# Optimization experiments

Measured on AMD Instinct MI355X. Metric: run time of the kernel, lower is better.

Reference implementation:

```python
import jax, jax.numpy as jnp
import numpy as np

T, H, I, E, K = 4096, 2048, 2048, 16, 4
EPS = 1e-6


def setup_inputs() -> dict:
    key = jax.random.key(0)
    ks = jax.random.split(key, 7)
    s = 0.02
    return {
        "x": jax.random.normal(ks[0], (T, H), dtype=jnp.float32),
        "gamma": jnp.ones((H,), dtype=jnp.float32),
        "wg": jax.random.normal(ks[1], (E, H), dtype=jnp.float32) * s,
        "bg": jax.random.normal(ks[2], (E,), dtype=jnp.float32) * s,
        "w1": jax.random.normal(ks[3], (E, I, H), dtype=jnp.float32) * s,  # gate proj
        "w3": jax.random.normal(ks[4], (E, I, H), dtype=jnp.float32) * s,  # up proj
        "w2": jax.random.normal(ks[5], (E, H, I), dtype=jnp.float32) * s,  # down proj
    }


def reference(x, gamma, wg, bg, w1, w3, w2):
    # RMSNorm
    t = x * jax.lax.rsqrt(jnp.mean(x * x, axis=-1, keepdims=True) + EPS) * gamma
    # Router: softmax -> top-k -> renormalize (FusedMoE renormalize=True)
    logits = t @ wg.T + bg                        # [T, E]
    probs = jax.nn.softmax(logits, axis=-1)
    vals, idx = jax.lax.top_k(probs, K)           # [T, K]
    vals = vals / jnp.sum(vals, axis=-1, keepdims=True)
    # Dense [T, E] routing-weight matrix (zeros outside top-k)
    route_w = jnp.einsum("tk,tke->te", vals, jax.nn.one_hot(idx, E, dtype=vals.dtype))
    # Grouped expert GEMMs: scan over experts, accumulate weighted outputs
    def body(acc, p):
        w1e, w3e, w2e, we = p                     # [I,H], [I,H], [H,I], [T]
        h = jax.nn.silu(t @ w1e.T) * (t @ w3e.T)  # [T, I]
        return acc + (h @ w2e.T) * we[:, None], None
    moe_out, _ = jax.lax.scan(body, jnp.zeros_like(x), (w1, w3, w2, route_w.T))
    return x + moe_out
```

## Files before the change

kernel.cpp:

```cpp
#include <hip/hip_runtime.h>
#include <hip/hip_bf16.h>

constexpr int TT = 4096;
constexpr int HH = 2048;
constexpr int II = 2048;
constexpr int EE = 16;
constexpr int KTOP = 4;

typedef __attribute__((ext_vector_type(4))) float f4;
typedef __attribute__((ext_vector_type(8))) short s8;

__device__ __forceinline__ short f2bf(float f) {
    union { __hip_bfloat16 b; short s; } u;
    u.b = __float2bfloat16(f);
    return u.s;
}
__device__ __forceinline__ float bf2f(short s) {
    union { unsigned u; float f; } v;
    v.u = ((unsigned)(unsigned short)s) << 16;
    return v.f;
}

__global__ void k_router(const float* __restrict__ x, const float* __restrict__ gamma,
                         const float* __restrict__ wg, const float* __restrict__ bg,
                         short* __restrict__ t16, int* __restrict__ cnt,
                         int* __restrict__ lst, float* __restrict__ lwt) {
    const int lane = threadIdx.x & 63;
    const int tok = blockIdx.x * 4 + (threadIdx.x >> 6);
    const float* xr = x + (size_t)tok * HH;
    float t[32];
    float ss = 0.f;
#pragma unroll
    for (int j = 0; j < 32; j++) { float v = xr[lane + 64 * j]; t[j] = v; ss += v * v; }
#pragma unroll
    for (int m = 32; m >= 1; m >>= 1) ss += __shfl_xor(ss, m);
    const float rs = rsqrtf(ss * (1.f / HH) + 1e-6f);
#pragma unroll
    for (int j = 0; j < 32; j++) t[j] *= rs * gamma[lane + 64 * j];

    short* tr = t16 + (size_t)tok * HH;
#pragma unroll
    for (int j = 0; j < 32; j++) tr[lane + 64 * j] = f2bf(t[j]);

    float logit[EE];
#pragma unroll
    for (int e = 0; e < EE; e++) {
        const float* wrow = wg + (size_t)e * HH;
        float a = 0.f;
#pragma unroll
        for (int j = 0; j < 32; j++) a += t[j] * wrow[lane + 64 * j];
#pragma unroll
        for (int m = 32; m >= 1; m >>= 1) a += __shfl_xor(a, m);
        logit[e] = a + bg[e];
    }
    unsigned chosen = 0u;
    int sel[KTOP]; float sv[KTOP];
#pragma unroll
    for (int k = 0; k < KTOP; k++) {
        float best = -1e30f; int bi = 0;
#pragma unroll
        for (int e = 0; e < EE; e++) {
            bool take = (!((chosen >> e) & 1u)) && (logit[e] > best);
            if (take) { best = logit[e]; bi = e; }
        }
        chosen |= 1u << bi; sel[k] = bi; sv[k] = best;
    }
    const float lmax = sv[0];
    float s = 0.f;
#pragma unroll
    for (int k = 0; k < KTOP; k++) { sv[k] = expf(sv[k] - lmax); s += sv[k]; }
    const float inv = 1.f / s;
    if (lane == 0) {
#pragma unroll
        for (int k = 0; k < KTOP; k++) {
            int e = sel[k];
            int p = atomicAdd(&cnt[e], 1);
            lst[e * TT + p] = tok * KTOP + k;
            lwt[e * TT + p] = sv[k] * inv;
        }
    }
}

__global__ __launch_bounds__(256, 2) void k_gemm_ffn_fused(
        const short* __restrict__ t16, const float* __restrict__ w1,
        const float* __restrict__ w3, short* __restrict__ h,
        const int* __restrict__ cnt, const int* __restrict__ lst) {
    const int e = blockIdx.z;
    const int Me = cnt[e];
    const int m0 = blockIdx.y * 128;
    if (m0 >= Me) return;
    const int n0 = blockIdx.x * 128;
    const float* we1 = w1 + (size_t)e * II * HH;
    const float* we3 = w3 + (size_t)e * II * HH;

    __shared__ char lA[16384];
    __shared__ char lB1[16384];
    __shared__ char lB2[16384];
    __shared__ int s_tok[128];

    const int tid = threadIdx.x;
    if (tid < 128) s_tok[tid] = (m0 + tid < Me) ? lst[e * TT + m0 + tid] : 0;
    __syncthreads();

    const int lane = tid & 63, wid = tid >> 6;
    const int wr = wid >> 1, wc = wid & 1;

    f4 acc1[4][4], acc2[4][4];
    const f4 zero = {0.f, 0.f, 0.f, 0.f};
#pragma unroll
    for (int i = 0; i < 4; i++)
#pragma unroll
        for (int j = 0; j < 4; j++) { acc1[i][j] = zero; acc2[i][j] = zero; }

    const int rbase = tid >> 3;
    const int kc = (tid & 7) * 8;
    const int lb0 = rbase * 128 + ((kc * 2) ^ ((rbase & 7) << 4));
    int tokrow[4];
#pragma unroll
    for (int j = 0; j < 4; j++) tokrow[j] = s_tok[rbase + 32 * j] >> 2;

    for (int kt = 0; kt < HH / 64; ++kt) {
        __syncthreads();
#pragma unroll
        for (int j = 0; j < 4; j++) {
            s8 av = *(const s8*)(t16 + (size_t)tokrow[j] * HH + kt * 64 + kc);
            *(s8*)(lA + lb0 + 4096 * j) = av;
        }
#pragma unroll
        for (int j = 0; j < 4; j++) {
            size_t roff = (size_t)(n0 + rbase + 32 * j) * HH + kt * 64 + kc;
            {
                f4 b0 = *(const f4*)(we1 + roff);
                f4 b1 = *(const f4*)(we1 + roff + 4);
                s8 bv;
#pragma unroll
                for (int i = 0; i < 4; i++) { bv[i] = f2bf(b0[i]); bv[4 + i] = f2bf(b1[i]); }
                *(s8*)(lB1 + lb0 + 4096 * j) = bv;
            }
            {
                f4 b0 = *(const f4*)(we3 + roff);
                f4 b1 = *(const f4*)(we3 + roff + 4);
                s8 bv;
#pragma unroll
                for (int i = 0; i < 4; i++) { bv[i] = f2bf(b0[i]); bv[4 + i] = f2bf(b1[i]); }
                *(s8*)(lB2 + lb0 + 4096 * j) = bv;
            }
        }
        __syncthreads();
#pragma unroll
        for (int kk = 0; kk < 2; ++kk) {
            s8 af[4], b1v[4], b2v[4];
#pragma unroll
            for (int mf = 0; mf < 4; mf++) {
                int r = wr * 64 + mf * 16 + (lane & 15);
                int byte = r * 128 + (((kk * 64) + ((lane >> 4) << 4)) ^ ((r & 7) << 4));
                af[mf] = *(const s8*)(lA + byte);
            }
#pragma unroll
            for (int nf = 0; nf < 4; nf++) {
                int r = wc * 64 + nf * 16 + (lane & 15);
                int byte = r * 128 + (((kk * 64) + ((lane >> 4) << 4)) ^ ((r & 7) << 4));
                b1v[nf] = *(const s8*)(lB1 + byte);
                b2v[nf] = *(const s8*)(lB2 + byte);
            }
#pragma unroll
            for (int mf = 0; mf < 4; mf++)
#pragma unroll
                for (int nf = 0; nf < 4; nf++) {
                    acc1[mf][nf] = __builtin_amdgcn_mfma_f32_16x16x32_bf16(
                        af[mf], b1v[nf], acc1[mf][nf], 0, 0, 0);
                    acc2[mf][nf] = __builtin_amdgcn_mfma_f32_16x16x32_bf16(
                        af[mf], b2v[nf], acc2[mf][nf], 0, 0, 0);
                }
        }
    }
#pragma unroll
    for (int mf = 0; mf < 4; mf++) {
#pragma unroll
        for (int j = 0; j < 4; j++) {
            int rl = wr * 64 + mf * 16 + ((lane >> 4) << 2) + j;
            if (m0 + rl < Me) {
                size_t orow = (size_t)s_tok[rl] * II;
#pragma unroll
                for (int nf = 0; nf < 4; nf++) {
                    int ncol = n0 + wc * 64 + nf * 16 + (lane & 15);
                    float g = acc1[mf][nf][j];
                    float u = acc2[mf][nf][j];
                    float sg = g / (1.f + expf(-g));
                    h[orow + ncol] = f2bf(sg * u);
                }
            }
        }
    }
}

__global__ __launch_bounds__(256, 2) void k_gemm_down(
        const short* __restrict__ h, const float* __restrict__ w2,
        short* __restrict__ buf2, const int* __restrict__ cnt,
        const int* __restrict__ lst, const float* __restrict__ lwt) {
    const int e = blockIdx.z;
    const int Me = cnt[e];
    const int m0 = blockIdx.y * 128;
    if (m0 >= Me) return;
    const int n0 = blockIdx.x * 128;
    const float* we = w2 + (size_t)e * HH * II;

    __shared__ char lA[16384];
    __shared__ char lB[16384];
    __shared__ int s_tok[128];
    __shared__ float s_wgt[128];

    const int tid = threadIdx.x;
    if (tid < 128) {
        bool v = (m0 + tid < Me);
        s_tok[tid] = v ? lst[e * TT + m0 + tid] : 0;
        s_wgt[tid] = v ? lwt[e * TT + m0 + tid] : 0.f;
    }
    __syncthreads();

    const int lane = tid & 63, wid = tid >> 6;
    const int wr = wid >> 1, wc = wid & 1;

    f4 acc[4][4];
    const f4 zero = {0.f, 0.f, 0.f, 0.f};
#pragma unroll
    for (int i = 0; i < 4; i++)
#pragma unroll
        for (int j = 0; j < 4; j++) acc[i][j] = zero;

    const int rbase = tid >> 3;
    const int kc = (tid & 7) * 8;
    const int lb0 = rbase * 128 + ((kc * 2) ^ ((rbase & 7) << 4));
    const short* gA[4]; const float* gB[4];
#pragma unroll
    for (int j = 0; j < 4; j++) {
        gA[j] = h + (size_t)s_tok[rbase + 32 * j] * II + kc;
        gB[j] = we + (size_t)(n0 + rbase + 32 * j) * II + kc;
    }

    s8 ar[4]; f4 br[4][2];
#define PREFETCH(kt)                                                           \
    _Pragma("unroll")                                                          \
    for (int j = 0; j < 4; j++) {                                              \
        ar[j] = *(const s8*)(gA[j] + (kt) * 64);                               \
        br[j][0] = *(const f4*)(gB[j] + (kt) * 64);                            \
        br[j][1] = *(const f4*)(gB[j] + (kt) * 64 + 4);                        \
    }

    PREFETCH(0);
    const int nkt = II / 64;
    for (int kt = 0; kt < nkt; ++kt) {
        asm volatile("" ::: "memory");
        __builtin_amdgcn_s_barrier();
        asm volatile("" ::: "memory");
#pragma unroll
        for (int j = 0; j < 4; j++) {
            *(s8*)(lA + lb0 + 4096 * j) = ar[j];
            s8 bv;
#pragma unroll
            for (int i = 0; i < 4; i++) { bv[i] = f2bf(br[j][0][i]); bv[4 + i] = f2bf(br[j][1][i]); }
            *(s8*)(lB + lb0 + 4096 * j) = bv;
        }
        if (kt + 1 < nkt) PREFETCH(kt + 1);
        asm volatile("s_waitcnt lgkmcnt(0)" ::: "memory");
        __builtin_amdgcn_s_barrier();
        asm volatile("" ::: "memory");
#pragma unroll
        for (int kk = 0; kk < 2; ++kk) {
            s8 af[4], bfr[4];
#pragma unroll
            for (int mf = 0; mf < 4; mf++) {
                int r = wr * 64 + mf * 16 + (lane & 15);
                int byte = r * 128 + (((kk * 64) + ((lane >> 4) << 4)) ^ ((r & 7) << 4));
                af[mf] = *(const s8*)(lA + byte);
            }
#pragma unroll
            for (int nf = 0; nf < 4; nf++) {
                int r = wc * 64 + nf * 16 + (lane & 15);
                int byte = r * 128 + (((kk * 64) + ((lane >> 4) << 4)) ^ ((r & 7) << 4));
                bfr[nf] = *(const s8*)(lB + byte);
            }
#pragma unroll
            for (int mf = 0; mf < 4; mf++)
#pragma unroll
                for (int nf = 0; nf < 4; nf++)
                    acc[mf][nf] = __builtin_amdgcn_mfma_f32_16x16x32_bf16(
                        af[mf], bfr[nf], acc[mf][nf], 0, 0, 0);
        }
    }
#undef PREFETCH
#pragma unroll
    for (int mf = 0; mf < 4; mf++) {
#pragma unroll
        for (int j = 0; j < 4; j++) {
            int rl = wr * 64 + mf * 16 + ((lane >> 4) << 2) + j;
            if (m0 + rl < Me) {
                size_t orow = (size_t)s_tok[rl] * HH;
                float wgt = s_wgt[rl];
#pragma unroll
                for (int nf = 0; nf < 4; nf++) {
                    int ncol = n0 + wc * 64 + nf * 16 + (lane & 15);
                    buf2[orow + ncol] = f2bf(acc[mf][nf][j] * wgt);
                }
            }
        }
    }
}

__global__ void k_final(const float* __restrict__ x, const short* __restrict__ buf2,
                        float* __restrict__ out) {
    size_t i8 = (size_t)blockIdx.x * 256 + threadIdx.x;
    size_t tok = i8 / (HH / 8);
    size_t c8 = i8 % (HH / 8);
    const f4* xp = (const f4*)x + i8 * 2;
    f4 r0 = xp[0], r1 = xp[1];
#pragma unroll
    for (int k = 0; k < KTOP; k++) {
        s8 b = ((const s8*)buf2)[(tok * KTOP + k) * (HH / 8) + c8];
#pragma unroll
        for (int j = 0; j < 4; j++) { r0[j] += bf2f(b[j]); r1[j] += bf2f(b[4 + j]); }
    }
    ((f4*)out)[i8 * 2] = r0;
    ((f4*)out)[i8 * 2 + 1] = r1;
}

extern "C" void kernel_launch(void* const* d_in, const int* in_sizes, int n_in,
                              void* d_out, int out_size, void* d_ws, size_t ws_size,
                              hipStream_t stream) {
    const float* x     = (const float*)d_in[0];
    const float* gamma = (const float*)d_in[1];
    const float* wg    = (const float*)d_in[2];
    const float* bg    = (const float*)d_in[3];
    const float* w1    = (const float*)d_in[4];
    const float* w3    = (const float*)d_in[5];
    const float* w2    = (const float*)d_in[6];
    float* out = (float*)d_out;

    char* ws = (char*)d_ws;
    size_t off = 0;
    short* t16  = (short*)(ws + off); off += (size_t)TT * HH * 2;
    short* h1   = (short*)(ws + off); off += (size_t)TT * KTOP * II * 2;
    short* buf2 = (short*)(ws + off); off += (size_t)TT * KTOP * HH * 2;
    int* cnt    = (int*)(ws + off); off += 256;
    int* lst    = (int*)(ws + off); off += (size_t)EE * TT * 4;
    float* lwt  = (float*)(ws + off); off += (size_t)EE * TT * 4;

    hipMemsetAsync(cnt, 0, EE * sizeof(int), stream);
    k_router<<<TT / 4, 256, 0, stream>>>(x, gamma, wg, bg, t16, cnt, lst, lwt);

    dim3 g1(II / 128, TT / 128, EE);
    k_gemm_ffn_fused<<<g1, 256, 0, stream>>>(t16, w1, w3, h1, cnt, lst);

    dim3 g2(HH / 128, TT / 128, EE);
    k_gemm_down<<<g2, 256, 0, stream>>>(h1, w2, buf2, cnt, lst, lwt);

    k_final<<<(TT * HH / 8) / 256, 256, 0, stream>>>(x, buf2, out);
}
```

Baseline: 912.4 us.

## Use direct global-to-LDS DMA with double buffering in both expert GEMMs

Both expert GEMM kernels now stage A and B tiles with global_load_lds (direct-to-LDS) into double-buffered shared memory, overlapping the next tile's load with MFMA work on the current one. The fp32 weights are kept as fp32 in LDS and converted to bf16 on fragment read instead of during staging. Output tiles shrink from 128 to 64 columns and K tiles from 64 to 32, and launch bounds rise to allow more resident blocks, with s_setprio raised around the MFMA section. The trade-off is more blocks and re-reads of the A tile, plus doubled LDS traffic for fp32 B and redundant bf16 conversion per wave.

Result: slower. 1.034 ms (+13.3%).

```diff
diff --git a/kernel.cpp b/kernel.cpp
--- a/kernel.cpp
+++ b/kernel.cpp
@@ -19,6 +19,12 @@
     union { unsigned u; float f; } v;
     v.u = ((unsigned)(unsigned short)s) << 16;
     return v.f;
+}
+
+__device__ __forceinline__ void g2l16(const void* g, void* l) {
+    __builtin_amdgcn_global_load_lds(
+        (const __attribute__((address_space(1))) void*)g,
+        (__attribute__((address_space(3))) void*)l, 16, 0, 0);
 }
 
 __global__ void k_router(const float* __restrict__ x, const float* __restrict__ gamma,
@@ -81,7 +87,7 @@
     }
 }
 
-__global__ __launch_bounds__(256, 2) void k_gemm_ffn_fused(
+__global__ __launch_bounds__(256, 3) void k_ffn(
         const short* __restrict__ t16, const float* __restrict__ w1,
         const float* __restrict__ w3, short* __restrict__ h,
         const int* __restrict__ cnt, const int* __restrict__ lst) {
@@ -89,91 +95,110 @@
     const int Me = cnt[e];
     const int m0 = blockIdx.y * 128;
     if (m0 >= Me) return;
-    const int n0 = blockIdx.x * 128;
+    const int n0 = blockIdx.x * 64;
     const float* we1 = w1 + (size_t)e * II * HH;
     const float* we3 = w3 + (size_t)e * II * HH;
 
-    __shared__ char lA[16384];
-    __shared__ char lB1[16384];
-    __shared__ char lB2[16384];
+    __shared__ short sA[2][128 * 32];
+    __shared__ float sB1[2][64 * 32];
+    __shared__ float sB2[2][64 * 32];
     __shared__ int s_tok[128];
 
     const int tid = threadIdx.x;
     if (tid < 128) s_tok[tid] = (m0 + tid < Me) ? lst[e * TT + m0 + tid] : 0;
     __syncthreads();
 
-    const int lane = tid & 63, wid = tid >> 6;
-    const int wr = wid >> 1, wc = wid & 1;
-
-    f4 acc1[4][4], acc2[4][4];
+    const int lane = tid & 63, w = tid >> 6;
+    const int wr = w >> 1, wc = w & 1;
+
+    const short* srcA[2]; const float* srcB1[2]; const float* srcB3[2];
+#pragma unroll
+    for (int i = 0; i < 2; i++) {
+        int Ra = (w * 2 + i) * 16 + (lane >> 2);
+        srcA[i] = t16 + (size_t)(s_tok[Ra] >> 2) * HH + ((lane & 3) ^ (Ra & 3)) * 8;
+        int Rb = (w * 2 + i) * 8 + (lane >> 3);
+        size_t ro = (size_t)(n0 + Rb) * HH + ((lane & 7) ^ (Rb & 7)) * 4;
+        srcB1[i] = we1 + ro;
+        srcB3[i] = we3 + ro;
+    }
+
+    f4 acc1[4][2], acc2[4][2];
     const f4 zero = {0.f, 0.f, 0.f, 0.f};
 #pragma unroll
     for (int i = 0; i < 4; i++)
 #pragma unroll
-        for (int j = 0; j < 4; j++) { acc1[i][j] = zero; acc2[i][j] = zero; }
-
-    const int rbase = tid >> 3;
-    const int kc = (tid & 7) * 8;
-    const int lb0 = rbase * 128 + ((kc * 2) ^ ((rbase & 7) << 4));
-    int tokrow[4];
-#pragma unroll
-    for (int j = 0; j < 4; j++) tokrow[j] = s_tok[rbase + 32 * j] >> 2;
-
-    for (int kt = 0; kt < HH / 64; ++kt) {
-        __syncthreads();
-#pragma unroll
-        for (int j = 0; j < 4; j++) {
-            s8 av = *(const s8*)(t16 + (size_t)tokrow[j] * HH + kt * 64 + kc);
-            *(s8*)(lA + lb0 + 4096 * j) = av;
-        }
-#pragma unroll
-        for (int j = 0; j < 4; j++) {
-            size_t roff = (size_t)(n0 + rbase + 32 * j) * HH + kt * 64 + kc;
-            {
-                f4 b0 = *(const f4*)(we1 + roff);
-                f4 b1 = *(const f4*)(we1 + roff + 4);
-                s8 bv;
-#pragma unroll
-                for (int i = 0; i < 4; i++) { bv[i] = f2bf(b0[i]); bv[4 + i] = f2bf(b1[i]); }
-                *(s8*)(lB1 + lb0 + 4096 * j) = bv;
+        for (int j = 0; j < 2; j++) { acc1[i][j] = zero; acc2[i][j] = zero; }
+
+#define DMA_TILE(db, kt)                                                       \
+    {                                                                          \
+        _Pragma("unroll")                                                      \
+        for (int i = 0; i < 2; i++)                                            \
+            g2l16(srcA[i] + (kt) * 32, (char*)sA[db] + (w * 2 + i) * 1024);    \
+        _Pragma("unroll")                                                      \
+        for (int i = 0; i < 2; i++)                                            \
+            g2l16(srcB1[i] + (kt) * 32, (char*)sB1[db] + (w * 2 + i) * 1024);  \
+        _Pragma("unroll")                                                      \
+        for (int i = 0; i < 2; i++)                                            \
+            g2l16(srcB3[i] + (kt) * 32, (char*)sB2[db] + (w * 2 + i) * 1024);  \
+    }
+
+    DMA_TILE(0, 0);
+    const int nkt = HH / 32;
+    for (int kt = 0; kt < nkt; ++kt) {
+        const int db = kt & 1;
+        if (kt + 1 < nkt) {
+            DMA_TILE(db ^ 1, kt + 1);
+            asm volatile("s_waitcnt vmcnt(6)" ::: "memory");
+        } else {
+            asm volatile("s_waitcnt vmcnt(0)" ::: "memory");
+        }
+        __builtin_amdgcn_s_barrier();
+        asm volatile("" ::: "memory");
+
+        s8 af[4];
+#pragma unroll
+        for (int mf = 0; mf < 4; mf++) {
+            int r = wr * 64 + mf * 16 + (lane & 15);
+            int byte = r * 64 + ((((lane >> 4) << 4)) ^ ((r & 3) << 4));
+            af[mf] = *(const s8*)((const char*)sA[db] + byte);
+        }
+        s8 b1v[2], b2v[2];
+#pragma unroll
+        for (int nf = 0; nf < 2; nf++) {
+            int r = wc * 32 + nf * 16 + (lane & 15);
+            int base = r * 128;
+            int o0 = ((lane >> 4) * 32) ^ ((r & 7) << 4);
+            int o1 = ((lane >> 4) * 32 + 16) ^ ((r & 7) << 4);
+            f4 x0 = *(const f4*)((const char*)sB1[db] + base + o0);
+            f4 x1 = *(const f4*)((const char*)sB1[db] + base + o1);
+            f4 y0 = *(const f4*)((const char*)sB2[db] + base + o0);
+            f4 y1 = *(const f4*)((const char*)sB2[db] + base + o1);
+            s8 bv1, bv2;
+#pragma unroll
+            for (int i = 0; i < 4; i++) {
+                bv1[i] = f2bf(x0[i]); bv1[4 + i] = f2bf(x1[i]);
+                bv2[i] = f2bf(y0[i]); bv2[4 + i] = f2bf(y1[i]);
             }
-            {
-                f4 b0 = *(const f4*)(we3 + roff);
-                f4 b1 = *(const f4*)(we3 + roff + 4);
-                s8 bv;
-#pragma unroll
-                for (int i = 0; i < 4; i++) { bv[i] = f2bf(b0[i]); bv[4 + i] = f2bf(b1[i]); }
-                *(s8*)(lB2 + lb0 + 4096 * j) = bv;
+            b1v[nf] = bv1; b2v[nf] = bv2;
+        }
+        __builtin_amdgcn_s_setprio(1);
+#pragma unroll
+        for (int mf = 0; mf < 4; mf++)
+#pragma unroll
+            for (int nf = 0; nf < 2; nf++) {
+                acc1[mf][nf] = __builtin_amdgcn_mfma_f32_16x16x32_bf16(
+                    af[mf], b1v[nf], acc1[mf][nf], 0, 0, 0);
+                acc2[mf][nf] = __builtin_amdgcn_mfma_f32_16x16x32_bf16(
+                    af[mf], b2v[nf], acc2[mf][nf], 0, 0, 0);
             }
-        }
-        __syncthreads();
-#pragma unroll
-        for (int kk = 0; kk < 2; ++kk) {
-            s8 af[4], b1v[4], b2v[4];
-#pragma unroll
-            for (int mf = 0; mf < 4; mf++) {
-                int r = wr * 64 + mf * 16 + (lane & 15);
-                int byte = r * 128 + (((kk * 64) + ((lane >> 4) << 4)) ^ ((r & 7) << 4));
-                af[mf] = *(const s8*)(lA + byte);
-            }
-#pragma unroll
-            for (int nf = 0; nf < 4; nf++) {
-                int r = wc * 64 + nf * 16 + (lane & 15);
-                int byte = r * 128 + (((kk * 64) + ((lane >> 4) << 4)) ^ ((r & 7) << 4));
-                b1v[nf] = *(const s8*)(lB1 + byte);
-                b2v[nf] = *(const s8*)(lB2 + byte);
-            }
-#pragma unroll
-            for (int mf = 0; mf < 4; mf++)
-#pragma unroll
-                for (int nf = 0; nf < 4; nf++) {
-                    acc1[mf][nf] = __builtin_amdgcn_mfma_f32_16x16x32_bf16(
-                        af[mf], b1v[nf], acc1[mf][nf], 0, 0, 0);
-                    acc2[mf][nf] = __builtin_amdgcn_mfma_f32_16x16x32_bf16(
-                        af[mf], b2v[nf], acc2[mf][nf], 0, 0, 0);
-                }
-        }
-    }
+        __builtin_amdgcn_s_setprio(0);
+
+        asm volatile("" ::: "memory");
+        __builtin_amdgcn_s_barrier();
+        asm volatile("" ::: "memory");
+    }
+#undef DMA_TILE
+
 #pragma unroll
     for (int mf = 0; mf < 4; mf++) {
 #pragma unroll
@@ -182,8 +207,8 @@
             if (m0 + rl < Me) {
                 size_t orow = (size_t)s_tok[rl] * II;
 #pragma unroll
-                for (int nf = 0; nf < 4; nf++) {
-                    int ncol = n0 + wc * 64 + nf * 16 + (lane & 15);
+                for (int nf = 0; nf < 2; nf++) {
+                    int ncol = n0 + wc * 32 + nf * 16 + (lane & 15);
                     float g = acc1[mf][nf][j];
                     float u = acc2[mf][nf][j];
                     float sg = g / (1.f + expf(-g));
@@ -194,7 +219,7 @@
     }
 }
 
-__global__ __launch_bounds__(256, 2) void k_gemm_down(
+__global__ __launch_bounds__(256, 4) void k_down(
         const short* __restrict__ h, const float* __restrict__ w2,
         short* __restrict__ buf2, const int* __restrict__ cnt,
         const int* __restrict__ lst, const float* __restrict__ lwt) {
@@ -202,11 +227,11 @@
     const int Me = cnt[e];
     const int m0 = blockIdx.y * 128;
     if (m0 >= Me) return;
-    const int n0 = blockIdx.x * 128;
+    const int n0 = blockIdx.x * 64;
     const float* we = w2 + (size_t)e * HH * II;
 
-    __shared__ char lA[16384];
-    __shared__ char lB[16384];
+    __shared__ short sA[2][128 * 32];
+    __shared__ float sB[2][64 * 32];
     __shared__ int s_tok[128];
     __shared__ float s_wgt[128];
 
@@ -218,77 +243,84 @@
     }
     __syncthreads();
 
-    const int lane = tid & 63, wid = tid >> 6;
-    const int wr = wid >> 1, wc = wid & 1;
-
-    f4 acc[4][4];
+    const int lane = tid & 63, w = tid >> 6;
+    const int wr = w >> 1, wc = w & 1;
+
+    const short* srcA[2]; const float* srcB[2];
+#pragma unroll
+    for (int i = 0; i < 2; i++) {
+        int Ra = (w * 2 + i) * 16 + (lane >> 2);
+        srcA[i] = h + (size_t)s_tok[Ra] * II + ((lane & 3) ^ (Ra & 3)) * 8;
+        int Rb = (w * 2 + i) * 8 + (lane >> 3);
+        srcB[i] = we + (size_t)(n0 + Rb) * II + ((lane & 7) ^ (Rb & 7)) * 4;
+    }
+
+    f4 acc[4][2];
     const f4 zero = {0.f, 0.f, 0.f, 0.f};
 #pragma unroll
     for (int i = 0; i < 4; i++)
 #pragma unroll
-        for (int j = 0; j < 4; j++) acc[i][j] = zero;
-
-    const int rbase = tid >> 3;
-    const int kc = (tid & 7) * 8;
-    const int lb0 = rbase * 128 + ((kc * 2) ^ ((rbase & 7) << 4));
-    const short* gA[4]; const float* gB[4];
-#pragma unroll
-    for (int j = 0; j < 4; j++) {
-        gA[j] = h + (size_t)s_tok[rbase + 32 * j] * II + kc;
-        gB[j] = we + (size_t)(n0 + rbase + 32 * j) * II + kc;
-    }
-
-    s8 ar[4]; f4 br[4][2];
-#define PREFETCH(kt)                                                           \
-    _Pragma("unroll")                                                          \
-    for (int j = 0; j < 4; j++) {                                              \
-        ar[j] = *(const s8*)(gA[j] + (kt) * 64);                               \
-        br[j][0] = *(const f4*)(gB[j] + (kt) * 64);                            \
-        br[j][1] = *(const f4*)(gB[j] + (kt) * 64 + 4);                        \
-    }
-
-    PREFETCH(0);
-    const int nkt = II / 64;
+        for (int j = 0; j < 2; j++) acc[i][j] = zero;
+
+#define DMA_TILE(db, kt)                                                       \
+    {                                                                          \
+        _Pragma("unroll")                                                      \
+        for (int i = 0; i < 2; i++)                                            \
+            g2l16(srcA[i] + (kt) * 32, (char*)sA[db] + (w * 2 + i) * 1024);    \
+        _Pragma("unroll")                                                      \
+        for (int i = 0; i < 2; i++)                                            \
+            g2l16(srcB[i] + (kt) * 32, (char*)sB[db] + (w * 2 + i) * 1024);    \
+    }
+
+    DMA_TILE(0, 0);
+    const int nkt = II / 32;
     for (int kt = 0; kt < nkt; ++kt) {
-        asm volatile("" ::: "memory");
+        const int db = kt & 1;
+        if (kt + 1 < nkt) {
+            DMA_TILE(db ^ 1, kt + 1);
+            asm volatile("s_waitcnt vmcnt(4)" ::: "memory");
+        } else {
+            asm volatile("s_waitcnt vmcnt(0)" ::: "memory");
+        }
         __builtin_amdgcn_s_barrier();
         asm volatile("" ::: "memory");
-#pragma unroll
-        for (int j = 0; j < 4; j++) {
-            *(s8*)(lA + lb0 + 4096 * j) = ar[j];
-            s8 bv;
-#pragma unroll
-            for (int i = 0; i < 4; i++) { bv[i] = f2bf(br[j][0][i]); bv[4 + i] = f2bf(br[j][1][i]); }
-            *(s8*)(lB + lb0 + 4096 * j) = bv;
-        }
-        if (kt + 1 < nkt) PREFETCH(kt + 1);
-        asm volatile("s_waitcnt lgkmcnt(0)" ::: "memory");
+
+        s8 af[4];
+#pragma unroll
+        for (int mf = 0; mf < 4; mf++) {
+            int r = wr * 64 + mf * 16 + (lane & 15);
+            int byte = r * 64 + ((((lane >> 4) << 4)) ^ ((r & 3) << 4));
+            af[mf] = *(const s8*)((const char*)sA[db] + byte);
+        }
+        s8 bv[2];
+#pragma unroll
+        for (int nf = 0; nf < 2; nf++) {
+            int r = wc * 32 + nf * 16 + (lane & 15);
+            int base = r * 128;
+            int o0 = ((lane >> 4) * 32) ^ ((r & 7) << 4);
+            int o1 = ((lane >> 4) * 32 + 16) ^ ((r & 7) << 4);
+            f4 x0 = *(const f4*)((const char*)sB[db] + base + o0);
+            f4 x1 = *(const f4*)((const char*)sB[db] + base + o1);
+            s8 b;
+#pragma unroll
+            for (int i = 0; i < 4; i++) { b[i] = f2bf(x0[i]); b[4 + i] = f2bf(x1[i]); }
+            bv[nf] = b;
+        }
+        __builtin_amdgcn_s_setprio(1);
+#pragma unroll
+        for (int mf = 0; mf < 4; mf++)
+#pragma unroll
+            for (int nf = 0; nf < 2; nf++)
+                acc[mf][nf] = __builtin_amdgcn_mfma_f32_16x16x32_bf16(
+                    af[mf], bv[nf], acc[mf][nf], 0, 0, 0);
+        __builtin_amdgcn_s_setprio(0);
+
+        asm volatile("" ::: "memory");
         __builtin_amdgcn_s_barrier();
         asm volatile("" ::: "memory");
-#pragma unroll
-        for (int kk = 0; kk < 2; ++kk) {
-            s8 af[4], bfr[4];
-#pragma unroll
-            for (int mf = 0; mf < 4; mf++) {
-                int r = wr * 64 + mf * 16 + (lane & 15);
-                int byte = r * 128 + (((kk * 64) + ((lane >> 4) << 4)) ^ ((r & 7) << 4));
-                af[mf] = *(const s8*)(lA + byte);
-            }
-#pragma unroll
-            for (int nf = 0; nf < 4; nf++) {
-                int r = wc * 64 + nf * 16 + (lane & 15);
-                int byte = r * 128 + (((kk * 64) + ((lane >> 4) << 4)) ^ ((r & 7) << 4));
-                bfr[nf] = *(const s8*)(lB + byte);
-            }
-#pragma unroll
-            for (int mf = 0; mf < 4; mf++)
-#pragma unroll
-                for (int nf = 0; nf < 4; nf++)
-                    acc[mf][nf] = __builtin_amdgcn_mfma_f32_16x16x32_bf16(
-                        af[mf], bfr[nf], acc[mf][nf], 0, 0, 0);
-        }
-    }
-#undef PREFETCH
+    }
+#undef DMA_TILE
+
 #pragma unroll
     for (int mf = 0; mf < 4; mf++) {
 #pragma unroll
@@ -298,8 +330,8 @@
                 size_t orow = (size_t)s_tok[rl] * HH;
                 float wgt = s_wgt[rl];
 #pragma unroll
-                for (int nf = 0; nf < 4; nf++) {
-                    int ncol = n0 + wc * 64 + nf * 16 + (lane & 15);
+                for (int nf = 0; nf < 2; nf++) {
+                    int ncol = n0 + wc * 32 + nf * 16 + (lane & 15);
                     buf2[orow + ncol] = f2bf(acc[mf][nf][j] * wgt);
                 }
             }
@@ -348,11 +380,11 @@
     hipMemsetAsync(cnt, 0, EE * sizeof(int), stream);
     k_router<<<TT / 4, 256, 0, stream>>>(x, gamma, wg, bg, t16, cnt, lst, lwt);
 
-    dim3 g1(II / 128, TT / 128, EE);
-    k_gemm_ffn_fused<<<g1, 256, 0, stream>>>(t16, w1, w3, h1, cnt, lst);
-
-    dim3 g2(HH / 128, TT / 128, EE);
-    k_gemm_down<<<g2, 256, 0, stream>>>(h1, w2, buf2, cnt, lst, lwt);
+    dim3 g1(II / 64, TT / 128, EE);
+    k_ffn<<<g1, 256, 0, stream>>>(t16, w1, w3, h1, cnt, lst);
+
+    dim3 g2(HH / 64, TT / 128, EE);
+    k_down<<<g2, 256, 0, stream>>>(h1, w2, buf2, cnt, lst, lwt);
 
     k_final<<<(TT * HH / 8) / 256, 256, 0, stream>>>(x, buf2, out);
 }
```
